# Kernel optimization log

Hardware: AMD Instinct MI355X
Metric: run time of the kernel (lower is better)

Reference implementation:

```python
import jax, jax.numpy as jnp
import numpy as np

T0 = 64    # coarse proposal intervals
TF = 128   # fine samples per ray


def contract(x):
    # mip-NeRF-360 style contraction with per-point max-coordinate scatter.
    ax = jnp.abs(x)
    mag = jnp.max(ax, axis=-1, keepdims=True)             # [..., 1]
    oh = jax.nn.one_hot(jnp.argmax(ax, axis=-1), x.shape[-1], dtype=x.dtype)
    scale = (1.0 - oh) / mag + oh * (2.0 - 1.0 / mag) / mag
    return jnp.where(mag < 1.0, x, x * scale)


def near_far_from_aabb(rays_o, rays_d, aabb, min_near=0.05):
    tmin = (aabb[:3] - rays_o) / (rays_d + 1e-15)
    tmax = (aabb[3:] - rays_o) / (rays_d + 1e-15)
    near = jnp.max(jnp.minimum(tmin, tmax), axis=-1, keepdims=True)
    far = jnp.min(jnp.maximum(tmin, tmax), axis=-1, keepdims=True)
    miss = far < near
    near = jnp.where(miss, 1e9, near)
    far = jnp.where(miss, 1e9, far)
    near = jnp.maximum(near, min_near)
    return near, far


def sample_pdf(bins, weights, T):
    # CDF inverse-transform sampling (no perturb), faithful to the torch helper.
    n_int = weights.shape[-1]
    w = weights + 0.01
    pdf = w / jnp.sum(w, axis=-1, keepdims=True)
    cdf = jnp.minimum(jnp.cumsum(pdf, axis=-1), 1.0)
    cdf = jnp.concatenate([jnp.zeros_like(cdf[..., :1]), cdf], axis=-1)  # [N, n_int+1]
    u = jnp.linspace(0.5 / T, 1.0 - 0.5 / T, T, dtype=bins.dtype)
    u = jnp.broadcast_to(u, (bins.shape[0], T))
    inds = jax.vmap(lambda c, uu: jnp.searchsorted(c, uu, side='right'))(cdf, u)
    below = jnp.clip(inds - 1, 0, n_int)
    above = jnp.clip(inds, 0, n_int)
    cdf0 = jnp.take_along_axis(cdf, below, axis=-1)
    cdf1 = jnp.take_along_axis(cdf, above, axis=-1)
    b0 = jnp.take_along_axis(bins, below, axis=-1)
    b1 = jnp.take_along_axis(bins, above, axis=-1)
    denom = cdf1 - cdf0
    t = jnp.clip(jnp.where(denom > 0, (u - cdf0) / jnp.maximum(denom, 1e-12), 0.0), 0.0, 1.0)
    return b0 + t * (b1 - b0)


def setup_inputs() -> dict:
    key = jax.random.key(0)
    k1, k2, k3, k4, k5 = jax.random.split(key, 5)
    N = 65536
    rays_o = (jax.random.uniform(k1, (N, 3), jnp.float32) - 0.5) * 1.0   # origins inside box
    d = jax.random.normal(k2, (N, 3), jnp.float32)
    rays_d = d / jnp.linalg.norm(d, axis=-1, keepdims=True)
    aabb = jnp.array([-2.0, -2.0, -2.0, 2.0, 2.0, 2.0], jnp.float32)
    weights_coarse = jax.random.uniform(k3, (N, T0), jnp.float32)
    sigmas = jax.random.uniform(k4, (N, TF), jnp.float32) * 20.0
    rgbs = jax.random.uniform(k5, (N, TF, 3), jnp.float32)
    return {"rays_o": rays_o, "rays_d": rays_d, "aabb": aabb,
            "weights_coarse": weights_coarse, "sigmas": sigmas, "rgbs": rgbs}


def reference(rays_o, rays_d, aabb, weights_coarse, sigmas, rgbs):
    N = rays_o.shape[0]
    # 1) ray-AABB intersection
    near, far = near_far_from_aabb(rays_o, rays_d, aabb)
    # 2) uniform coarse bins in [near, far]
    s = jnp.linspace(0.0, 1.0, T0 + 1, dtype=rays_o.dtype)
    bins = near + (far - near) * s                              # [N, T0+1]
    # 3) CDF inverse-sample TF+1 fine bin edges from proposal weights
    z_edges = sample_pdf(bins, weights_coarse, TF + 1)          # [N, TF+1]
    deltas = z_edges[..., 1:] - z_edges[..., :-1]               # [N, TF]
    z = 0.5 * (z_edges[..., 1:] + z_edges[..., :-1])            # [N, TF]
    # 4) sample positions + contraction warp
    xyzs = rays_o[:, None, :] + rays_d[:, None, :] * z[..., None]  # [N, TF, 3]
    xyzs_c = contract(xyzs)
    # 5) alpha compositing
    alphas = 1.0 - jnp.exp(-sigmas * deltas)                    # [N, TF]
    trans = jnp.cumprod(
        jnp.concatenate([jnp.ones_like(alphas[..., :1]), 1.0 - alphas + 1e-10], axis=-1),
        axis=-1)[..., :-1]
    w = alphas * trans                                          # [N, TF]
    image = jnp.sum(w[..., None] * rgbs, axis=1)                # [N, 3]
    depth = jnp.sum(w * z, axis=-1, keepdims=True)              # [N, 1]
    return jnp.concatenate([image, depth, xyzs_c.reshape(N, -1)], axis=-1)  # [N, 4+3*TF]
```

## Files before the change

### kernel.cpp

```cpp
#include <hip/hip_runtime.h>
#include <hip/hip_bf16.h>


constexpr int kT0 = 64;
constexpr int kTF = 128;

__global__ __launch_bounds__(128)
void nerf_render_kernel(const float* __restrict__ rays_o,
                        const float* __restrict__ rays_d,
                        const float* __restrict__ aabb,
                        const float* __restrict__ weights,
                        const float* __restrict__ sigmas,
                        const float* __restrict__ rgbs,
                        float* __restrict__ out)
{
    const int ray  = blockIdx.x;
    const int tid  = threadIdx.x;
    const int lane = tid & 63;
    const int wid  = tid >> 6;

    __shared__ float s_cdf[kT0 + 1];
    __shared__ float s_zedge[kTF + 1];
    __shared__ float s_rgb[kTF * 3];
    __shared__ float s_xyz[kTF * 3];
    __shared__ float s_red[8];
    __shared__ float s_wavetot;

    const float* rgb_row = rgbs + (size_t)ray * (kTF * 3);
    #pragma unroll
    for (int k = 0; k < 3; ++k) s_rgb[tid + 128 * k] = rgb_row[tid + 128 * k];

    const float ox = rays_o[ray * 3 + 0], oy = rays_o[ray * 3 + 1], ozr = rays_o[ray * 3 + 2];
    const float dx = rays_d[ray * 3 + 0], dy = rays_d[ray * 3 + 1], dzr = rays_d[ray * 3 + 2];
    float near, far;
    {
        const float t0x = (aabb[0] - ox) / (dx + 1e-15f);
        const float t1x = (aabb[3] - ox) / (dx + 1e-15f);
        const float t0y = (aabb[1] - oy) / (dy + 1e-15f);
        const float t1y = (aabb[4] - oy) / (dy + 1e-15f);
        const float t0z = (aabb[2] - ozr) / (dzr + 1e-15f);
        const float t1z = (aabb[5] - ozr) / (dzr + 1e-15f);
        near = fmaxf(fmaxf(fminf(t0x, t1x), fminf(t0y, t1y)), fminf(t0z, t1z));
        far  = fminf(fminf(fmaxf(t0x, t1x), fmaxf(t0y, t1y)), fmaxf(t0z, t1z));
        if (far < near) { near = 1e9f; far = 1e9f; }
        near = fmaxf(near, 0.05f);
    }
    const float range = far - near;

    if (wid == 0) {
        float w = weights[(size_t)ray * kT0 + lane] + 0.01f;
        float scan = w;
        #pragma unroll
        for (int off = 1; off < 64; off <<= 1) {
            float v = __shfl_up(scan, off);
            if (lane >= off) scan += v;
        }
        const float total = __shfl(scan, 63);
        s_cdf[lane + 1] = fminf(scan / total, 1.0f);
        if (lane == 0) s_cdf[0] = 0.0f;
    }
    __syncthreads();

    for (int j = tid; j <= kTF; j += 128) {
        const float u = ((float)j + 0.5f) / (float)(kTF + 1);
        int lo = 0, hi = kT0 + 1;
        while (lo < hi) {
            const int mid = (lo + hi) >> 1;
            if (s_cdf[mid] <= u) lo = mid + 1; else hi = mid;
        }
        int below = lo - 1; below = below < 0 ? 0 : (below > kT0 ? kT0 : below);
        int above = lo;     above = above > kT0 ? kT0 : above;
        const float c0 = s_cdf[below], c1 = s_cdf[above];
        const float b0 = near + range * ((float)below * (1.0f / kT0));
        const float b1 = near + range * ((float)above * (1.0f / kT0));
        const float denom = c1 - c0;
        float t = 0.0f;
        if (denom > 0.0f)
            t = fminf(fmaxf((u - c0) / fmaxf(denom, 1e-12f), 0.0f), 1.0f);
        s_zedge[j] = b0 + t * (b1 - b0);
    }
    __syncthreads();

    const float ze0 = s_zedge[tid], ze1 = s_zedge[tid + 1];
    const float delta = ze1 - ze0;
    const float z = 0.5f * (ze0 + ze1);
    const float sigma = sigmas[(size_t)ray * kTF + tid];
    const float e = expf(-sigma * delta);
    const float alpha = 1.0f - e;
    const float f = (1.0f - alpha) + 1e-10f;

    float scan = f;
    #pragma unroll
    for (int off = 1; off < 64; off <<= 1) {
        float v = __shfl_up(scan, off);
        if (lane >= off) scan *= v;
    }
    float excl = __shfl_up(scan, 1);
    if (lane == 0) excl = 1.0f;
    if (tid == 63) s_wavetot = scan;
    __syncthreads();
    const float trans = (wid == 0) ? excl : s_wavetot * excl;
    const float w = alpha * trans;

    float vr = w * s_rgb[3 * tid + 0];
    float vg = w * s_rgb[3 * tid + 1];
    float vb = w * s_rgb[3 * tid + 2];
    float vd = w * z;
    #pragma unroll
    for (int off = 32; off >= 1; off >>= 1) {
        vr += __shfl_down(vr, off);
        vg += __shfl_down(vg, off);
        vb += __shfl_down(vb, off);
        vd += __shfl_down(vd, off);
    }
    if (lane == 0) {
        s_red[wid * 4 + 0] = vr; s_red[wid * 4 + 1] = vg;
        s_red[wid * 4 + 2] = vb; s_red[wid * 4 + 3] = vd;
    }

    float px = ox  + dx  * z;
    float py = oy  + dy  * z;
    float pz = ozr + dzr * z;
    const float ax = fabsf(px), ay = fabsf(py), az = fabsf(pz);
    float mag; int idx;
    if (ax >= ay && ax >= az) { mag = ax; idx = 0; }
    else if (ay >= az)        { mag = ay; idx = 1; }
    else                      { mag = az; idx = 2; }
    if (mag >= 1.0f) {
        const float inv  = 1.0f / mag;
        const float smax = (2.0f - inv) * inv;
        px *= (idx == 0) ? smax : inv;
        py *= (idx == 1) ? smax : inv;
        pz *= (idx == 2) ? smax : inv;
    }
    s_xyz[3 * tid + 0] = px;
    s_xyz[3 * tid + 1] = py;
    s_xyz[3 * tid + 2] = pz;
    __syncthreads();

    float* orow = out + (size_t)ray * (4 + kTF * 3);
    if (tid == 0) {
        orow[0] = s_red[0] + s_red[4];
        orow[1] = s_red[1] + s_red[5];
        orow[2] = s_red[2] + s_red[6];
        orow[3] = s_red[3] + s_red[7];
    }
    #pragma unroll
    for (int k = 0; k < 3; ++k) {
        const int i = tid + 128 * k;
        orow[4 + i] = s_xyz[i];
    }
}

extern "C" void kernel_launch(void* const* d_in, const int* in_sizes, int n_in,
                              void* d_out, int out_size, void* d_ws, size_t ws_size,
                              hipStream_t stream) {
    const float* rays_o  = (const float*)d_in[0];
    const float* rays_d  = (const float*)d_in[1];
    const float* aabb    = (const float*)d_in[2];
    const float* weights = (const float*)d_in[3];
    const float* sigmas  = (const float*)d_in[4];
    const float* rgbs    = (const float*)d_in[5];
    float* out           = (float*)d_out;

    const int N = in_sizes[0] / 3;
    nerf_render_kernel<<<N, 128, 0, stream>>>(rays_o, rays_d, aabb, weights, sigmas, rgbs, out);
}
```

Baseline: 257.3 us.

## Map one wavefront per ray and scatter CDF intervals instead of binary search

Restructures the kernel so each 64-lane wavefront handles one ray, four rays per 256-thread block, with two fine samples per lane. The shared-memory rgb staging, the cross-wave transmittance combine and most block barriers go away. The per-sample binary search is replaced by each coarse interval writing the fine edges that fall inside it, and the divisions become fast reciprocal and exp intrinsics. This reduces synchronisation and redundant work, but global loads and stores become strided per lane and precision may differ slightly. The launch assumes N is divisible by four, and the scatter-inverted CDF may handle edge cases such as zero-width intervals differently.

```diff
diff --git a/kernel.cpp b/kernel.cpp
--- a/kernel.cpp
+++ b/kernel.cpp
@@ -1,11 +1,11 @@
 #include <hip/hip_runtime.h>
-#include <hip/hip_bf16.h>
 
 
 constexpr int kT0 = 64;
 constexpr int kTF = 128;
+constexpr int kRaysPerBlock = 4;
 
-__global__ __launch_bounds__(128)
+__global__ __launch_bounds__(256)
 void nerf_render_kernel(const float* __restrict__ rays_o,
                         const float* __restrict__ rays_d,
                         const float* __restrict__ aabb,
@@ -14,32 +14,22 @@
                         const float* __restrict__ rgbs,
                         float* __restrict__ out)
 {
-    const int ray  = blockIdx.x;
-    const int tid  = threadIdx.x;
-    const int lane = tid & 63;
-    const int wid  = tid >> 6;
+    const int lane = threadIdx.x & 63;
+    const int wid  = threadIdx.x >> 6;
+    const int ray  = blockIdx.x * kRaysPerBlock + wid;
 
-    __shared__ float s_cdf[kT0 + 1];
-    __shared__ float s_zedge[kTF + 1];
-    __shared__ float s_rgb[kTF * 3];
-    __shared__ float s_xyz[kTF * 3];
-    __shared__ float s_red[8];
-    __shared__ float s_wavetot;
-
-    const float* rgb_row = rgbs + (size_t)ray * (kTF * 3);
-    #pragma unroll
-    for (int k = 0; k < 3; ++k) s_rgb[tid + 128 * k] = rgb_row[tid + 128 * k];
+    __shared__ float s_zedge[kRaysPerBlock][kTF + 1];
 
     const float ox = rays_o[ray * 3 + 0], oy = rays_o[ray * 3 + 1], ozr = rays_o[ray * 3 + 2];
     const float dx = rays_d[ray * 3 + 0], dy = rays_d[ray * 3 + 1], dzr = rays_d[ray * 3 + 2];
     float near, far;
     {
-        const float t0x = (aabb[0] - ox) / (dx + 1e-15f);
-        const float t1x = (aabb[3] - ox) / (dx + 1e-15f);
-        const float t0y = (aabb[1] - oy) / (dy + 1e-15f);
-        const float t1y = (aabb[4] - oy) / (dy + 1e-15f);
-        const float t0z = (aabb[2] - ozr) / (dzr + 1e-15f);
-        const float t1z = (aabb[5] - ozr) / (dzr + 1e-15f);
+        const float rx = __builtin_amdgcn_rcpf(dx + 1e-15f);
+        const float ry = __builtin_amdgcn_rcpf(dy + 1e-15f);
+        const float rz = __builtin_amdgcn_rcpf(dzr + 1e-15f);
+        const float t0x = (aabb[0] - ox) * rx, t1x = (aabb[3] - ox) * rx;
+        const float t0y = (aabb[1] - oy) * ry, t1y = (aabb[4] - oy) * ry;
+        const float t0z = (aabb[2] - ozr) * rz, t1z = (aabb[5] - ozr) * rz;
         near = fmaxf(fmaxf(fminf(t0x, t1x), fminf(t0y, t1y)), fminf(t0z, t1z));
         far  = fminf(fminf(fmaxf(t0x, t1x), fmaxf(t0y, t1y)), fmaxf(t0z, t1z));
         if (far < near) { near = 1e9f; far = 1e9f; }
@@ -47,65 +37,68 @@
     }
     const float range = far - near;
 
-    if (wid == 0) {
-        float w = weights[(size_t)ray * kT0 + lane] + 0.01f;
-        float scan = w;
-        #pragma unroll
-        for (int off = 1; off < 64; off <<= 1) {
-            float v = __shfl_up(scan, off);
-            if (lane >= off) scan += v;
+    float wgt = weights[(size_t)ray * kT0 + lane] + 0.01f;
+    float scan = wgt;
+    #pragma unroll
+    for (int off = 1; off < 64; off <<= 1) {
+        float v = __shfl_up(scan, off);
+        if (lane >= off) scan += v;
+    }
+    const float total = __shfl(scan, 63);
+    const float c_hi_raw = fminf(scan * __builtin_amdgcn_rcpf(total), 1.0f);
+    float c_lo = __shfl_up(c_hi_raw, 1);
+    if (lane == 0) c_lo = 0.0f;
+    const float c_hi = c_hi_raw;
+
+    {
+        const float b_lo = near + range * ((float)lane * (1.0f / kT0));
+        const float b_hi = near + range * ((float)(lane + 1) * (1.0f / kT0));
+        const float bw = b_hi - b_lo;
+        int j_start = (int)ceilf(fmaf(129.0f, c_lo, -0.5f));
+        int j_end   = (int)ceilf(fmaf(129.0f, c_hi, -0.5f));
+        j_start = j_start < 0 ? 0 : j_start;
+        j_end   = j_end > (kTF + 1) ? (kTF + 1) : j_end;
+        const float rdenom = __builtin_amdgcn_rcpf(c_hi - c_lo);
+        for (int j = j_start; j < j_end; ++j) {
+            const float u = ((float)j + 0.5f) * (1.0f / 129.0f);
+            float t = (u - c_lo) * rdenom;
+            t = fminf(fmaxf(t, 0.0f), 1.0f);
+            s_zedge[wid][j] = fmaf(t, bw, b_lo);
         }
-        const float total = __shfl(scan, 63);
-        s_cdf[lane + 1] = fminf(scan / total, 1.0f);
-        if (lane == 0) s_cdf[0] = 0.0f;
     }
     __syncthreads();
 
-    for (int j = tid; j <= kTF; j += 128) {
-        const float u = ((float)j + 0.5f) / (float)(kTF + 1);
-        int lo = 0, hi = kT0 + 1;
-        while (lo < hi) {
-            const int mid = (lo + hi) >> 1;
-            if (s_cdf[mid] <= u) lo = mid + 1; else hi = mid;
-        }
-        int below = lo - 1; below = below < 0 ? 0 : (below > kT0 ? kT0 : below);
-        int above = lo;     above = above > kT0 ? kT0 : above;
-        const float c0 = s_cdf[below], c1 = s_cdf[above];
-        const float b0 = near + range * ((float)below * (1.0f / kT0));
-        const float b1 = near + range * ((float)above * (1.0f / kT0));
-        const float denom = c1 - c0;
-        float t = 0.0f;
-        if (denom > 0.0f)
-            t = fminf(fmaxf((u - c0) / fmaxf(denom, 1e-12f), 0.0f), 1.0f);
-        s_zedge[j] = b0 + t * (b1 - b0);
-    }
-    __syncthreads();
+    const float ze0 = s_zedge[wid][2 * lane + 0];
+    const float ze1 = s_zedge[wid][2 * lane + 1];
+    const float ze2 = s_zedge[wid][2 * lane + 2];
+    const float d0 = ze1 - ze0, d1 = ze2 - ze1;
+    const float z0 = 0.5f * (ze0 + ze1), z1 = 0.5f * (ze1 + ze2);
 
-    const float ze0 = s_zedge[tid], ze1 = s_zedge[tid + 1];
-    const float delta = ze1 - ze0;
-    const float z = 0.5f * (ze0 + ze1);
-    const float sigma = sigmas[(size_t)ray * kTF + tid];
-    const float e = expf(-sigma * delta);
-    const float alpha = 1.0f - e;
-    const float f = (1.0f - alpha) + 1e-10f;
+    const float2 sg = *(const float2*)(sigmas + (size_t)ray * kTF + 2 * lane);
+    const float e0 = __expf(-sg.x * d0);
+    const float e1 = __expf(-sg.y * d1);
+    const float a0 = 1.0f - e0, a1 = 1.0f - e1;
+    const float f0 = (1.0f - a0) + 1e-10f;
+    const float f1 = (1.0f - a1) + 1e-10f;
 
-    float scan = f;
+    float p = f0 * f1;
     #pragma unroll
     for (int off = 1; off < 64; off <<= 1) {
-        float v = __shfl_up(scan, off);
-        if (lane >= off) scan *= v;
+        float v = __shfl_up(p, off);
+        if (lane >= off) p *= v;
     }
-    float excl = __shfl_up(scan, 1);
+    float excl = __shfl_up(p, 1);
     if (lane == 0) excl = 1.0f;
-    if (tid == 63) s_wavetot = scan;
-    __syncthreads();
-    const float trans = (wid == 0) ? excl : s_wavetot * excl;
-    const float w = alpha * trans;
+    const float tr0 = excl;
+    const float tr1 = excl * f0;
+    const float w0 = a0 * tr0;
+    const float w1 = a1 * tr1;
 
-    float vr = w * s_rgb[3 * tid + 0];
-    float vg = w * s_rgb[3 * tid + 1];
-    float vb = w * s_rgb[3 * tid + 2];
-    float vd = w * z;
+    const float* rgb_row = rgbs + (size_t)ray * (kTF * 3) + 6 * lane;
+    float vr = w0 * rgb_row[0] + w1 * rgb_row[3];
+    float vg = w0 * rgb_row[1] + w1 * rgb_row[4];
+    float vb = w0 * rgb_row[2] + w1 * rgb_row[5];
+    float vd = w0 * z0 + w1 * z1;
     #pragma unroll
     for (int off = 32; off >= 1; off >>= 1) {
         vr += __shfl_down(vr, off);
@@ -113,42 +106,32 @@
         vb += __shfl_down(vb, off);
         vd += __shfl_down(vd, off);
     }
+
+    float* orow = out + (size_t)ray * (4 + kTF * 3);
     if (lane == 0) {
-        s_red[wid * 4 + 0] = vr; s_red[wid * 4 + 1] = vg;
-        s_red[wid * 4 + 2] = vb; s_red[wid * 4 + 3] = vd;
+        orow[0] = vr; orow[1] = vg; orow[2] = vb; orow[3] = vd;
     }
 
-    float px = ox  + dx  * z;
-    float py = oy  + dy  * z;
-    float pz = ozr + dzr * z;
-    const float ax = fabsf(px), ay = fabsf(py), az = fabsf(pz);
-    float mag; int idx;
-    if (ax >= ay && ax >= az) { mag = ax; idx = 0; }
-    else if (ay >= az)        { mag = ay; idx = 1; }
-    else                      { mag = az; idx = 2; }
-    if (mag >= 1.0f) {
-        const float inv  = 1.0f / mag;
-        const float smax = (2.0f - inv) * inv;
-        px *= (idx == 0) ? smax : inv;
-        py *= (idx == 1) ? smax : inv;
-        pz *= (idx == 2) ? smax : inv;
-    }
-    s_xyz[3 * tid + 0] = px;
-    s_xyz[3 * tid + 1] = py;
-    s_xyz[3 * tid + 2] = pz;
-    __syncthreads();
-
-    float* orow = out + (size_t)ray * (4 + kTF * 3);
-    if (tid == 0) {
-        orow[0] = s_red[0] + s_red[4];
-        orow[1] = s_red[1] + s_red[5];
-        orow[2] = s_red[2] + s_red[6];
-        orow[3] = s_red[3] + s_red[7];
-    }
     #pragma unroll
-    for (int k = 0; k < 3; ++k) {
-        const int i = tid + 128 * k;
-        orow[4 + i] = s_xyz[i];
+    for (int s = 0; s < 2; ++s) {
+        const float z = s ? z1 : z0;
+        float px = ox  + dx  * z;
+        float py = oy  + dy  * z;
+        float pz = ozr + dzr * z;
+        const float ax = fabsf(px), ay = fabsf(py), az = fabsf(pz);
+        float mag; int idx;
+        if (ax >= ay && ax >= az) { mag = ax; idx = 0; }
+        else if (ay >= az)        { mag = ay; idx = 1; }
+        else                      { mag = az; idx = 2; }
+        if (mag >= 1.0f) {
+            const float inv  = __builtin_amdgcn_rcpf(mag);
+            const float smax = (2.0f - inv) * inv;
+            px *= (idx == 0) ? smax : inv;
+            py *= (idx == 1) ? smax : inv;
+            pz *= (idx == 2) ? smax : inv;
+        }
+        float* o = orow + 4 + 6 * lane + 3 * s;
+        o[0] = px; o[1] = py; o[2] = pz;
     }
 }
 
@@ -164,5 +147,6 @@
     float* out           = (float*)d_out;
 
     const int N = in_sizes[0] / 3;
-    nerf_render_kernel<<<N, 128, 0, stream>>>(rays_o, rays_d, aabb, weights, sigmas, rgbs, out);
+    const int blocks = N / kRaysPerBlock;
+    nerf_render_kernel<<<blocks, 256, 0, stream>>>(rays_o, rays_d, aabb, weights, sigmas, rgbs, out);
 }
```

Result: faster. 222.2 us (-13.6%).
